# Optimization experiments

Hardware: AMD Instinct MI355X
Metric: run time of the kernel (lower is better)

Reference implementation:

```python
import jax, jax.numpy as jnp
import numpy as np

B, L, IDIM = 1, 1024, 2048
H, DK, DV, K = 16, 128, 128, 4
KEY_DIM = H * DK          # 2048
VAL_DIM = H * DV          # 2048
CONV_DIM = 2 * KEY_DIM + VAL_DIM  # 6144
EPS = 1e-6


def setup_inputs() -> dict:
    key = jax.random.key(0)
    ks = jax.random.split(key, 8)
    s = 0.02
    x = jax.random.normal(ks[0], (B, L, IDIM), jnp.float32)
    Wqkv = jax.random.normal(ks[1], (IDIM, CONV_DIM), jnp.float32) * s
    Wz = jax.random.normal(ks[2], (IDIM, VAL_DIM), jnp.float32) * s
    Wb = jax.random.normal(ks[3], (IDIM, H), jnp.float32) * s
    Wa = jax.random.normal(ks[4], (IDIM, H), jnp.float32) * s
    conv_w = jax.random.normal(ks[5], (CONV_DIM, 1, K), jnp.float32) * 0.2  # depthwise [O,I/g=1,K]
    A_log = jnp.log(jax.random.uniform(ks[6], (H,), jnp.float32, 0.1, 16.0))
    dt_bias = jnp.ones((H,), jnp.float32)
    norm_w = jnp.ones((DV,), jnp.float32)
    Wout = jax.random.normal(ks[7], (VAL_DIM, IDIM), jnp.float32) * s
    return dict(x=x, Wqkv=Wqkv, Wz=Wz, Wb=Wb, Wa=Wa, conv_w=conv_w,
                A_log=A_log, dt_bias=dt_bias, norm_w=norm_w, Wout=Wout)


def _l2norm(t):
    return t * jax.lax.rsqrt(jnp.sum(t * t, axis=-1, keepdims=True) + EPS)


def reference(x, Wqkv, Wz, Wb, Wa, conv_w, A_log, dt_bias, norm_w, Wout):
    b, l, _ = x.shape
    # fused QKV projection + causal depthwise conv + SiLU
    qkv = jnp.einsum('bld,dc->blc', x, Wqkv)                 # [B,L,CONV_DIM]
    qkv = jnp.transpose(qkv, (0, 2, 1))                      # [B,C,L]
    qkv = jax.lax.conv_general_dilated(
        qkv, conv_w, window_strides=(1,), padding=[(K - 1, 0)],
        dimension_numbers=('NCL', 'OIL', 'NCL'), feature_group_count=CONV_DIM)
    qkv = jax.nn.silu(jnp.transpose(qkv, (0, 2, 1)))         # [B,L,C]
    q, k, v = jnp.split(qkv, [KEY_DIM, 2 * KEY_DIM], axis=-1)

    z = jnp.einsum('bld,dv->blv', x, Wz)                     # [B,L,VAL_DIM]
    beta = jax.nn.sigmoid(jnp.einsum('bld,dh->blh', x, Wb))  # [B,L,H]
    A = -jnp.exp(A_log)                                      # [H]
    dt = jax.nn.softplus(jnp.einsum('bld,dh->blh', x, Wa) + dt_bias)
    g = dt * A                                               # [B,L,H] (negative)

    q = _l2norm(q.reshape(b, l, H, DK))
    k = _l2norm(k.reshape(b, l, H, DK))
    v = v.reshape(b, l, H, DV)
    scale = DK ** -0.5

    # time-major for scan: [L,B,H,...]
    qs = jnp.transpose(q, (1, 0, 2, 3)) * scale
    ks_ = jnp.transpose(k, (1, 0, 2, 3))
    vs = jnp.transpose(v, (1, 0, 2, 3))
    bs = jnp.transpose(beta, (1, 0, 2))
    gs = jnp.transpose(g, (1, 0, 2))

    M0 = jnp.zeros((b, H, DK, DV), jnp.float32)

    def step(M, inp):
        q_t, k_t, v_t, b_t, g_t = inp
        M = M * jnp.exp(g_t)[..., None, None]                    # decay
        Mk = jnp.einsum('bhd,bhdv->bhv', k_t, M)                 # readout of old mem
        M = M + jnp.einsum('bhd,bhv->bhdv', k_t, (v_t - Mk) * b_t[..., None])
        o_t = jnp.einsum('bhd,bhdv->bhv', q_t, M)
        return M, o_t

    _, out = jax.lax.scan(step, M0, (qs, ks_, vs, bs, gs))   # out: [L,B,H,DV]
    out = jnp.transpose(out, (1, 0, 2, 3))                   # [B,L,H,DV]

    # RMSNormGated: rms_norm(o) * weight * silu(z)
    zg = z.reshape(b, l, H, DV)
    rms = jax.lax.rsqrt(jnp.mean(out * out, axis=-1, keepdims=True) + EPS)
    out = (out * rms) * norm_w * jax.nn.silu(zg)

    out = out.reshape(b, l, VAL_DIM)
    return jnp.einsum('blv,vd->bld', out, Wout)
```

## Files before the change

### kernel.cpp

```cpp
#include <hip/hip_runtime.h>

typedef short bf16x8 __attribute__((ext_vector_type(8)));
typedef float f32x4 __attribute__((ext_vector_type(4)));
typedef float f32x2 __attribute__((ext_vector_type(2)));
typedef unsigned short u16;
typedef u16 u16x4 __attribute__((ext_vector_type(4)));

#define L_SEQ 1024
#define IDIM_ 2048
#define H_ 16
#define DK_ 128
#define DV_ 128
#define KEYD 2048
#define VALD 2048
#define CONVD 6144
#define QZD 8192
#define CH 16
#define NCH (L_SEQ / CH)
#define SCH 64
#define NSC (L_SEQ / SCH)

__device__ __forceinline__ u16 f2bf(float f) {
  union { float f; unsigned u; } v; v.f = f;
  unsigned r = v.u + 0x7FFF + ((v.u >> 16) & 1);
  return (u16)(r >> 16);
}

__device__ __forceinline__ float red16(float x) {
  union U { float f; int i; } a, t;
  a.f = x;
  t.i = __builtin_amdgcn_update_dpp(0, a.i, 0xB1, 0xF, 0xF, true); a.f += t.f;
  t.i = __builtin_amdgcn_update_dpp(0, a.i, 0x4E, 0xF, 0xF, true); a.f += t.f;
  t.i = __builtin_amdgcn_update_dpp(0, a.i, 0x141, 0xF, 0xF, true); a.f += t.f;
  t.i = __builtin_amdgcn_update_dpp(0, a.i, 0x140, 0xF, 0xF, true); a.f += t.f;
  return a.f;
}

__device__ __forceinline__ void gl_lds16(const float* g, float* l) {
  __builtin_amdgcn_global_load_lds(
      (const __attribute__((address_space(1))) void*)g,
      (__attribute__((address_space(3))) void*)l, 16, 0, 0);
}
__device__ __forceinline__ void gl_lds4(const float* g, float* l) {
  __builtin_amdgcn_global_load_lds(
      (const __attribute__((address_space(1))) void*)g,
      (__attribute__((address_space(3))) void*)l, 4, 0, 0);
}

__global__ __launch_bounds__(256) void prepcast_kernel(const float* __restrict__ x,
                                                       const float* __restrict__ Wqkv,
                                                       const float* __restrict__ Wz,
                                                       const float* __restrict__ Wout,
                                                       u16* __restrict__ xb,
                                                       u16* __restrict__ WcatT,
                                                       u16* __restrict__ WoutT) {
  __shared__ float tile[32][33];
  const int bid = blockIdx.x;
  if (bid < 2048) {
    int i = (bid * 256 + threadIdx.x) * 4;
    f32x4 v = *(const f32x4*)&x[i];
    u16x4 o = { f2bf(v[0]), f2bf(v[1]), f2bf(v[2]), f2bf(v[3]) };
    *(u16x4*)&xb[i] = o;
    return;
  }
  const float* W; u16* WT; int R, C, bx, by;
  if (bid < 14336) {
    int t = bid - 2048;  bx = t % 192; by = t / 192;
    W = Wqkv; WT = WcatT; R = IDIM_; C = CONVD;
  } else if (bid < 18432) {
    int t = bid - 14336; bx = t & 63; by = t >> 6;
    W = Wz; WT = WcatT + (size_t)CONVD * IDIM_; R = IDIM_; C = VALD;
  } else {
    int t = bid - 18432; bx = t & 63; by = t >> 6;
    W = Wout; WT = WoutT; R = VALD; C = IDIM_;
  }
  int c0 = bx * 32, r0 = by * 32;
  int tx = threadIdx.x & 31, ty = threadIdx.x >> 5;
#pragma unroll
  for (int j = 0; j < 4; ++j)
    tile[ty + j * 8][tx] = W[(size_t)(r0 + ty + j * 8) * C + c0 + tx];
  __syncthreads();
#pragma unroll
  for (int j = 0; j < 4; ++j)
    WT[(size_t)(c0 + ty + j * 8) * R + r0 + tx] = f2bf(tile[tx][ty + j * 8]);
}

__global__ __launch_bounds__(256) void gemm_bt_kernel(const u16* __restrict__ A,
                                                      const u16* __restrict__ B,
                                                      float* __restrict__ C,
                                                      int M, int N, int K) {
  __shared__ short As[128 * 72];
  __shared__ short Bs[128 * 72];
  const int tid = threadIdx.x;
  const int lane = tid & 63, wave = tid >> 6;
  const int wm = wave >> 1, wn = wave & 1;
  const int m0 = blockIdx.y * 128, n0 = blockIdx.x * 128;
  const int l15 = lane & 15, lhi = lane >> 4;

  f32x4 acc[4][4] = {};

  for (int k0 = 0; k0 < K; k0 += 64) {
    __syncthreads();
#pragma unroll
    for (int i = 0; i < 4; ++i) {
      int chunk = tid + i * 256;
      int row = chunk >> 3;
      int kc = (chunk & 7) * 8;
      *(bf16x8*)&As[row * 72 + kc] =
          *(const bf16x8*)&A[(size_t)(m0 + row) * K + k0 + kc];
      *(bf16x8*)&Bs[row * 72 + kc] =
          *(const bf16x8*)&B[(size_t)(n0 + row) * K + k0 + kc];
    }
    __syncthreads();
#pragma unroll
    for (int kk = 0; kk < 64; kk += 32) {
      const int koff = kk + lhi * 8;
      bf16x8 a[4], b[4];
#pragma unroll
      for (int m = 0; m < 4; ++m)
        a[m] = *(const bf16x8*)&As[(wm * 64 + m * 16 + l15) * 72 + koff];
#pragma unroll
      for (int n = 0; n < 4; ++n)
        b[n] = *(const bf16x8*)&Bs[(wn * 64 + n * 16 + l15) * 72 + koff];
#pragma unroll
      for (int m = 0; m < 4; ++m)
#pragma unroll
        for (int n = 0; n < 4; ++n)
          acc[m][n] = __builtin_amdgcn_mfma_f32_16x16x32_bf16(a[m], b[n], acc[m][n], 0, 0, 0);
    }
  }
#pragma unroll
  for (int m = 0; m < 4; ++m)
#pragma unroll
    for (int n = 0; n < 4; ++n)
#pragma unroll
      for (int j = 0; j < 4; ++j) {
        int row = m0 + wm * 64 + m * 16 + lhi * 4 + j;
        int col = n0 + wn * 64 + n * 16 + l15;
        C[(size_t)row * N + col] = acc[m][n][j];
      }
}

__global__ __launch_bounds__(256) void gemm_bt64_kernel(const u16* __restrict__ A,
                                                        const u16* __restrict__ B,
                                                        float* __restrict__ C,
                                                        int M, int N, int K) {
  __shared__ short As[64 * 72];
  __shared__ short Bs[128 * 72];
  const int tid = threadIdx.x;
  const int lane = tid & 63, wave = tid >> 6;
  const int wm = wave >> 1, wn = wave & 1;
  const int m0 = blockIdx.y * 64, n0 = blockIdx.x * 128;
  const int l15 = lane & 15, lhi = lane >> 4;

  f32x4 acc[2][4] = {};

  for (int k0 = 0; k0 < K; k0 += 64) {
    __syncthreads();
#pragma unroll
    for (int i = 0; i < 2; ++i) {
      int chunk = tid + i * 256;
      int row = chunk >> 3;
      int kc = (chunk & 7) * 8;
      *(bf16x8*)&As[row * 72 + kc] =
          *(const bf16x8*)&A[(size_t)(m0 + row) * K + k0 + kc];
    }
#pragma unroll
    for (int i = 0; i < 4; ++i) {
      int chunk = tid + i * 256;
      int row = chunk >> 3;
      int kc = (chunk & 7) * 8;
      *(bf16x8*)&Bs[row * 72 + kc] =
          *(const bf16x8*)&B[(size_t)(n0 + row) * K + k0 + kc];
    }
    __syncthreads();
#pragma unroll
    for (int kk = 0; kk < 64; kk += 32) {
      const int koff = kk + lhi * 8;
      bf16x8 a[2], b[4];
#pragma unroll
      for (int m = 0; m < 2; ++m)
        a[m] = *(const bf16x8*)&As[(wm * 32 + m * 16 + l15) * 72 + koff];
#pragma unroll
      for (int n = 0; n < 4; ++n)
        b[n] = *(const bf16x8*)&Bs[(wn * 64 + n * 16 + l15) * 72 + koff];
#pragma unroll
      for (int m = 0; m < 2; ++m)
#pragma unroll
        for (int n = 0; n < 4; ++n)
          acc[m][n] = __builtin_amdgcn_mfma_f32_16x16x32_bf16(a[m], b[n], acc[m][n], 0, 0, 0);
    }
  }
#pragma unroll
  for (int m = 0; m < 2; ++m)
#pragma unroll
    for (int n = 0; n < 4; ++n)
#pragma unroll
      for (int j = 0; j < 4; ++j) {
        int row = m0 + wm * 32 + m * 16 + lhi * 4 + j;
        int col = n0 + wn * 64 + n * 16 + l15;
        C[(size_t)row * N + col] = acc[m][n][j];
      }
}

__global__ __launch_bounds__(128) void betag_kernel(const float* __restrict__ x,
                                                    const float* __restrict__ Wb,
                                                    const float* __restrict__ Wa,
                                                    const float* __restrict__ A_log,
                                                    const float* __restrict__ dt_bias,
                                                    float* __restrict__ btT,
                                                    float* __restrict__ egT,
                                                    float* __restrict__ gT) {
  int l = blockIdx.x;
  __shared__ float xs[IDIM_];
  __shared__ float redb[128], reda[128];
  for (int i = threadIdx.x; i < IDIM_; i += 128) xs[i] = x[(size_t)l * IDIM_ + i];
  __syncthreads();
  int h = threadIdx.x & 15, part = threadIdx.x >> 4;
  float sb = 0.f, sa = 0.f;
  int d0 = part * 256;
  for (int d = d0; d < d0 + 256; ++d) {
    float xv = xs[d];
    sb += xv * Wb[d * 16 + h];
    sa += xv * Wa[d * 16 + h];
  }
  redb[threadIdx.x] = sb;
  reda[threadIdx.x] = sa;
  __syncthreads();
  if (threadIdx.x < 16) {
    float b = 0.f, a = 0.f;
#pragma unroll
    for (int p = 0; p < 8; ++p) { b += redb[p * 16 + h]; a += reda[p * 16 + h]; }
    btT[h * L_SEQ + l] = 1.f / (1.f + expf(-b));
    float dtv = a + dt_bias[h];
    dtv = (dtv > 20.f) ? dtv : log1pf(expf(dtv));
    float g = -expf(A_log[h]) * dtv;
    egT[h * L_SEQ + l] = expf(g);
    gT[h * L_SEQ + l] = g;
  }
}

__global__ __launch_bounds__(256) void prep2_kernel(const float* __restrict__ qkvz,
                                                    const float* __restrict__ cw,
                                                    float* __restrict__ qn,
                                                    float* __restrict__ kn,
                                                    float* __restrict__ vT) {
  __shared__ float tile[32][33];
  const int bid = blockIdx.x;
  if (bid < 4096) {
    int wid = bid * 4 + (threadIdx.x >> 6);
    int lane = threadIdx.x & 63;
    int l = wid >> 4, h = wid & 15;
    const int cq = h * 128 + lane * 2;
    const int ck = KEYD + cq;
    const float* row0 = qkvz + (size_t)l * QZD;
    f32x4 wq0 = *(const f32x4*)&cw[cq * 4];
    f32x4 wq1 = *(const f32x4*)&cw[(cq + 1) * 4];
    f32x4 wk0 = *(const f32x4*)&cw[ck * 4];
    f32x4 wk1 = *(const f32x4*)&cw[(ck + 1) * 4];
    f32x2 xq = *(const f32x2*)&row0[cq];
    f32x2 xk = *(const f32x2*)&row0[ck];
    float q0 = xq[0] * wq0[3], q1 = xq[1] * wq1[3];
    float k0 = xk[0] * wk0[3], k1 = xk[1] * wk1[3];
    if (l >= 1) {
      f32x2 aq = *(const f32x2*)&row0[cq - QZD];
      f32x2 ak = *(const f32x2*)&row0[ck - QZD];
      q0 += aq[0] * wq0[2]; q1 += aq[1] * wq1[2];
      k0 += ak[0] * wk0[2]; k1 += ak[1] * wk1[2];
    }
    if (l >= 2) {
      f32x2 aq = *(const f32x2*)&row0[cq - 2 * QZD];
      f32x2 ak = *(const f32x2*)&row0[ck - 2 * QZD];
      q0 += aq[0] * wq0[1]; q1 += aq[1] * wq1[1];
      k0 += ak[0] * wk0[1]; k1 += ak[1] * wk1[1];
    }
    if (l >= 3) {
      f32x2 aq = *(const f32x2*)&row0[cq - 3 * QZD];
      f32x2 ak = *(const f32x2*)&row0[ck - 3 * QZD];
      q0 += aq[0] * wq0[0]; q1 += aq[1] * wq1[0];
      k0 += ak[0] * wk0[0]; k1 += ak[1] * wk1[0];
    }
    f32x2 qv = { q0 / (1.f + expf(-q0)), q1 / (1.f + expf(-q1)) };
    f32x2 kv = { k0 / (1.f + expf(-k0)), k1 / (1.f + expf(-k1)) };

    float ssq = qv[0] * qv[0] + qv[1] * qv[1];
    float ssk = kv[0] * kv[0] + kv[1] * kv[1];
#pragma unroll
    for (int s = 1; s < 64; s <<= 1) {
      ssq += __shfl_xor(ssq, s);
      ssk += __shfl_xor(ssk, s);
    }
    float scq = 0.08838834764831845f / sqrtf(ssq + 1e-6f);
    float sck = 1.f / sqrtf(ssk + 1e-6f);
    qv[0] *= scq; qv[1] *= scq;
    kv[0] *= sck; kv[1] *= sck;
    size_t base = ((size_t)h * L_SEQ + l) * 128 + lane * 2;
    *(f32x2*)&qn[base] = qv;
    *(f32x2*)&kn[base] = kv;
    return;
  }
  int t = bid - 4096;
  int c0 = (t & 63) * 32, l0 = (t >> 6) * 32;
  int tx = threadIdx.x & 31, ty = threadIdx.x >> 5;
  const int c = 2 * KEYD + c0 + tx;
  f32x4 w = *(const f32x4*)&cw[c * 4];
#pragma unroll
  for (int j = 0; j < 4; ++j) {
    int l = l0 + ty + j * 8;
    const float* p = qkvz + (size_t)l * QZD + c;
    float s = p[0] * w[3];
    if (l >= 1) s += p[-QZD] * w[2];
    if (l >= 2) s += p[-2 * QZD] * w[1];
    if (l >= 3) s += p[-3 * QZD] * w[0];
    tile[ty + j * 8][tx] = s / (1.f + expf(-s));
  }
  __syncthreads();
#pragma unroll
  for (int j = 0; j < 4; ++j)
    vT[(size_t)(c0 + ty + j * 8) * L_SEQ + l0 + tx] = tile[tx][ty + j * 8];
}

__global__ __launch_bounds__(256) void scan_kernel(const float* __restrict__ kn,
                                                   const float* __restrict__ vT,
                                                   const float* __restrict__ egT,
                                                   const float* __restrict__ btT,
                                                   float* __restrict__ Mb,
                                                   float* __restrict__ DbT) {
  __shared__ alignas(16) float ks[2][CH][128];
  __shared__ alignas(16) float vs[2][16][CH];
  __shared__ alignas(16) float ebc[2][2][CH];

  const int tid = threadIdx.x;
  const int wave = tid >> 6, lane = tid & 63;
  const int dk_sub = lane & 15;
  const int head = blockIdx.x & 15;
  const int dv0 = (blockIdx.x >> 4) * 16;
  const int col_local = tid >> 4;
  const int dv = dv0 + col_local;

  const float* kh = kn + (size_t)head * L_SEQ * 128;

  auto stage = [&](int chunk, int buf) {
    const int l0 = chunk * CH;
    const float* kg = kh + (size_t)l0 * 128;
#pragma unroll
    for (int i = 0; i < 2; ++i) {
      int seg = i * 4 + wave;
      int off = seg * 256 + lane * 4;
      gl_lds16(kg + off, &ks[buf][0][0] + seg * 256);
    }
    {
      int idx = wave * 64 + lane;
      gl_lds4(vT + (size_t)(head * 128 + dv0 + (idx >> 4)) * L_SEQ + l0 + (idx & 15),
              &vs[buf][0][0] + wave * 64);
    }
    if (wave == 0 && lane < 32) {
      const float* src = (lane < 16) ? (egT + head * L_SEQ + l0 + lane)
                                     : (btT + head * L_SEQ + l0 + (lane - 16));
      gl_lds4(src, &ebc[buf][0][0]);
    }
  };

  stage(0, 0);
  __syncthreads();

  f32x4 Mlo = {0.f, 0.f, 0.f, 0.f}, Mhi = {0.f, 0.f, 0.f, 0.f};
  const int dkb = dk_sub * 8;
  float* dcol = DbT + (size_t)(head * 128 + dv) * L_SEQ;

#pragma unroll 1
  for (int c = 0; c < NCH; ++c) {
    const int buf = c & 1;
    if (c + 1 < NCH) stage(c + 1, buf ^ 1);

    if ((c & 3) == 0) {
      int sc = c >> 2;
      float* mrow = Mb + (((size_t)sc * 16 + head) * 128 + dv) * 128 + dkb;
      *(f32x4*)mrow = Mlo;
      *(f32x4*)(mrow + 4) = Mhi;
    }

    f32x4 ev[4], bv[4], vv[4];
#pragma unroll
    for (int i = 0; i < 4; ++i) {
      ev[i] = *(const f32x4*)&ebc[buf][0][i * 4];
      bv[i] = *(const f32x4*)&ebc[buf][1][i * 4];
      vv[i] = *(const f32x4*)&vs[buf][col_local][i * 4];
    }
    f32x4 kr[4][2];
#pragma unroll
    for (int i = 0; i < 3; ++i) {
      kr[i][0] = *(const f32x4*)&ks[buf][i][dkb];
      kr[i][1] = *(const f32x4*)&ks[buf][i][dkb + 4];
    }

#pragma unroll
    for (int s = 0; s < CH; ++s) {
      if (s + 3 < CH) {
        kr[(s + 3) & 3][0] = *(const f32x4*)&ks[buf][s + 3][dkb];
        kr[(s + 3) & 3][1] = *(const f32x4*)&ks[buf][s + 3][dkb + 4];
      }
      const f32x4 k0 = kr[s & 3][0], k1 = kr[s & 3][1];
      const float e = ev[s >> 2][s & 3], b = bv[s >> 2][s & 3];
      const float v = vv[s >> 2][s & 3];

      float skm0 = k0[0] * Mlo[0], skm1 = k0[1] * Mlo[1];
      skm0 = fmaf(k0[2], Mlo[2], skm0); skm1 = fmaf(k0[3], Mlo[3], skm1);
      skm0 = fmaf(k1[0], Mhi[0], skm0); skm1 = fmaf(k1[1], Mhi[1], skm1);
      skm0 = fmaf(k1[2], Mhi[2], skm0); skm1 = fmaf(k1[3], Mhi[3], skm1);
      f32x4 emlo, emhi;
#pragma unroll
      for (int i = 0; i < 4; ++i) { emlo[i] = e * Mlo[i]; emhi[i] = e * Mhi[i]; }
      float skm = red16(skm0 + skm1);
      float dl = (v - e * skm) * b;
      if (dk_sub == 0) dcol[c * CH + s] = dl;
#pragma unroll
      for (int i = 0; i < 4; ++i) {
        Mlo[i] = fmaf(k0[i], dl, emlo[i]);
        Mhi[i] = fmaf(k1[i], dl, emhi[i]);
      }
    }
    __syncthreads();
  }
}

__global__ __launch_bounds__(256) void opass_kernel(const float* __restrict__ qn,
                                                    const float* __restrict__ kn,
                                                    const float* __restrict__ DbT,
                                                    const float* __restrict__ gT,
                                                    const float* __restrict__ Mb,
                                                    float* __restrict__ oatt) {
  __shared__ alignas(16) u16 qsb[64][136];
  __shared__ alignas(16) u16 bbuf[128][136];
  __shared__ alignas(16) u16 Asb[64][72];
  __shared__ float gsh[64], Gh[64];

  const int tid = threadIdx.x;
  const int lane = tid & 63, wave = tid >> 6;
  const int l15 = lane & 15, lhi = lane >> 4;
  const int h = blockIdx.x & 15, sc = blockIdx.x >> 4;
  const int l0 = sc * SCH;

  {
    int t = tid >> 2, c0 = (tid & 3) * 32;
    const float* qr = qn + ((size_t)h * L_SEQ + l0 + t) * 128 + c0;
    const float* kr = kn + ((size_t)h * L_SEQ + l0 + t) * 128 + c0;
#pragma unroll
    for (int j = 0; j < 8; ++j) {
      f32x4 vq = *(const f32x4*)&qr[j * 4];
      f32x4 vk = *(const f32x4*)&kr[j * 4];
      u16x4 oq = { f2bf(vq[0]), f2bf(vq[1]), f2bf(vq[2]), f2bf(vq[3]) };
      u16x4 ok = { f2bf(vk[0]), f2bf(vk[1]), f2bf(vk[2]), f2bf(vk[3]) };
      *(u16x4*)&qsb[t][c0 + j * 4] = oq;
      *(u16x4*)&bbuf[t][c0 + j * 4] = ok;
    }
  }
  if (tid < 64) gsh[tid] = gT[h * L_SEQ + l0 + tid];
  __syncthreads();
  if (tid < 64) {
    float a = 0.f;
    for (int u = 0; u <= tid; ++u) a += gsh[u];
    Gh[tid] = a;
  }
  __syncthreads();

  f32x4 acc1[2][2] = {};
  const int wm = wave >> 1, wn = wave & 1;
#pragma unroll
  for (int kk = 0; kk < 128; kk += 32) {
    const int koff = kk + lhi * 8;
    bf16x8 a[2], b[2];
#pragma unroll
    for (int m = 0; m < 2; ++m)
      a[m] = *(const bf16x8*)&qsb[wm * 32 + m * 16 + l15][koff];
#pragma unroll
    for (int n = 0; n < 2; ++n)
      b[n] = *(const bf16x8*)&bbuf[wn * 32 + n * 16 + l15][koff];
#pragma unroll
    for (int m = 0; m < 2; ++m)
#pragma unroll
      for (int n = 0; n < 2; ++n)
        acc1[m][n] = __builtin_amdgcn_mfma_f32_16x16x32_bf16(a[m], b[n], acc1[m][n], 0, 0, 0);
  }
#pragma unroll
  for (int m = 0; m < 2; ++m)
#pragma unroll
    for (int n = 0; n < 2; ++n)
#pragma unroll
      for (int j = 0; j < 4; ++j) {
        int t = wm * 32 + m * 16 + lhi * 4 + j;
        int s = wn * 32 + n * 16 + l15;
        float a = (s <= t) ? acc1[m][n][j] * expf(Gh[t] - Gh[s]) : 0.f;
        Asb[t][s] = f2bf(a);
      }
  __syncthreads();

  {
    int dv = tid >> 1, c0 = (tid & 1) * 64;
    const float* mr = Mb + (((size_t)sc * 16 + h) * 128 + dv) * 128 + c0;
#pragma unroll
    for (int j = 0; j < 16; ++j) {
      f32x4 v = *(const f32x4*)&mr[j * 4];
      u16x4 o = { f2bf(v[0]), f2bf(v[1]), f2bf(v[2]), f2bf(v[3]) };
      *(u16x4*)&bbuf[dv][c0 + j * 4] = o;
    }
  }
  __syncthreads();

  f32x4 acc[2][4] = {};
#pragma unroll
  for (int kk = 0; kk < 128; kk += 32) {
    const int koff = kk + lhi * 8;
    bf16x8 a[2], b[4];
#pragma unroll
    for (int m = 0; m < 2; ++m)
      a[m] = *(const bf16x8*)&qsb[wm * 32 + m * 16 + l15][koff];
#pragma unroll
    for (int n = 0; n < 4; ++n)
      b[n] = *(const bf16x8*)&bbuf[wn * 64 + n * 16 + l15][koff];
#pragma unroll
    for (int m = 0; m < 2; ++m)
#pragma unroll
      for (int n = 0; n < 4; ++n)
        acc[m][n] = __builtin_amdgcn_mfma_f32_16x16x32_bf16(a[m], b[n], acc[m][n], 0, 0, 0);
  }
#pragma unroll
  for (int m = 0; m < 2; ++m) {
#pragma unroll
    for (int j = 0; j < 4; ++j) {
      int t = wm * 32 + m * 16 + lhi * 4 + j;
      float sc1 = expf(Gh[t]);
#pragma unroll
      for (int n = 0; n < 4; ++n) acc[m][n][j] *= sc1;
    }
  }
  __syncthreads();

  {
    int dv = tid >> 1, c0 = (tid & 1) * 32;
    const float* dr = DbT + (size_t)(h * 128 + dv) * L_SEQ + l0 + c0;
#pragma unroll
    for (int j = 0; j < 8; ++j) {
      f32x4 v = *(const f32x4*)&dr[j * 4];
      u16x4 o = { f2bf(v[0]), f2bf(v[1]), f2bf(v[2]), f2bf(v[3]) };
      *(u16x4*)&bbuf[dv][c0 + j * 4] = o;
    }
  }
  __syncthreads();

#pragma unroll
  for (int kk = 0; kk < 64; kk += 32) {
    const int koff = kk + lhi * 8;
    bf16x8 a[2], b[4];
#pragma unroll
    for (int m = 0; m < 2; ++m)
      a[m] = *(const bf16x8*)&Asb[wm * 32 + m * 16 + l15][koff];
#pragma unroll
    for (int n = 0; n < 4; ++n)
      b[n] = *(const bf16x8*)&bbuf[wn * 64 + n * 16 + l15][koff];
#pragma unroll
    for (int m = 0; m < 2; ++m)
#pragma unroll
      for (int n = 0; n < 4; ++n)
        acc[m][n] = __builtin_amdgcn_mfma_f32_16x16x32_bf16(a[m], b[n], acc[m][n], 0, 0, 0);
  }

#pragma unroll
  for (int m = 0; m < 2; ++m)
#pragma unroll
    for (int n = 0; n < 4; ++n)
#pragma unroll
      for (int j = 0; j < 4; ++j) {
        int t = wm * 32 + m * 16 + lhi * 4 + j;
        int dv = wn * 64 + n * 16 + l15;
        oatt[((size_t)(l0 + t) * 16 + h) * 128 + dv] = acc[m][n][j];
      }
}

__global__ __launch_bounds__(256) void grms_kernel(const float* __restrict__ oatt,
                                                   const float* __restrict__ qkvz,
                                                   const float* __restrict__ norm_w,
                                                   u16* __restrict__ gn) {
  int wid = blockIdx.x * 4 + (threadIdx.x >> 6);
  int lane = threadIdx.x & 63;
  int l = wid >> 4, h = wid & 15;
  const float* o = oatt + (size_t)wid * 128;
  f32x2 ov = *(const f32x2*)&o[lane * 2];
  float ss = ov[0] * ov[0] + ov[1] * ov[1];
#pragma unroll
  for (int s = 1; s < 64; s <<= 1) ss += __shfl_xor(ss, s);
  float r = 1.f / sqrtf(ss * (1.f / 128.f) + 1e-6f);
  const float* zp = qkvz + (size_t)l * QZD + CONVD + h * 128;
  f32x2 zv = *(const f32x2*)&zp[lane * 2];
  u16 r0, r1;
  {
    float sil = zv[0] / (1.f + expf(-zv[0]));
    r0 = f2bf(ov[0] * r * norm_w[lane * 2] * sil);
    float sil1 = zv[1] / (1.f + expf(-zv[1]));
    r1 = f2bf(ov[1] * r * norm_w[lane * 2 + 1] * sil1);
  }
  u16* dst = gn + (size_t)l * VALD + h * 128 + lane * 2;
  dst[0] = r0; dst[1] = r1;
}

extern "C" void kernel_launch(void* const* d_in, const int* in_sizes, int n_in,
                              void* d_out, int out_size, void* d_ws, size_t ws_size,
                              hipStream_t stream) {
  const float* x      = (const float*)d_in[0];
  const float* Wqkv   = (const float*)d_in[1];
  const float* Wz     = (const float*)d_in[2];
  const float* Wb     = (const float*)d_in[3];
  const float* Wa     = (const float*)d_in[4];
  const float* conv_w = (const float*)d_in[5];
  const float* A_log  = (const float*)d_in[6];
  const float* dt_bias= (const float*)d_in[7];
  const float* norm_w = (const float*)d_in[8];
  const float* Wout   = (const float*)d_in[9];
  float* out = (float*)d_out;

  char* ws = (char*)d_ws;
  size_t off = 0;
  auto alloc = [&](size_t bytes) {
    void* p = ws + off;
    off = (off + bytes + 255) & ~(size_t)255;
    return p;
  };
  u16* xb     = (u16*)alloc((size_t)L_SEQ * IDIM_ * 2);
  u16* WcatT  = (u16*)alloc((size_t)QZD * IDIM_ * 2);
  u16* WoutT  = (u16*)alloc((size_t)IDIM_ * VALD * 2);
  float* qkvz = (float*)alloc((size_t)L_SEQ * QZD * 4);
  float* qn   = (float*)alloc((size_t)H_ * L_SEQ * 128 * 4);
  float* kn   = (float*)alloc((size_t)H_ * L_SEQ * 128 * 4);
  float* vT   = (float*)alloc((size_t)H_ * 128 * L_SEQ * 4);
  float* btT  = (float*)alloc((size_t)L_SEQ * H_ * 4);
  float* egT  = (float*)alloc((size_t)L_SEQ * H_ * 4);
  float* gTb  = (float*)alloc((size_t)L_SEQ * H_ * 4);
  float* Mb   = (float*)alloc((size_t)NSC * H_ * 128 * 128 * 4);
  float* DbT  = (float*)alloc((size_t)H_ * 128 * L_SEQ * 4);
  float* oatt = (float*)alloc((size_t)L_SEQ * H_ * DV_ * 4);
  u16* gn     = (u16*)alloc((size_t)L_SEQ * VALD * 2);

  prepcast_kernel<<<22528, 256, 0, stream>>>(x, Wqkv, Wz, Wout, xb, WcatT, WoutT);

  gemm_bt_kernel<<<dim3(QZD / 128, L_SEQ / 128), 256, 0, stream>>>(xb, WcatT, qkvz, L_SEQ, QZD, IDIM_);

  betag_kernel<<<L_SEQ, 128, 0, stream>>>(x, Wb, Wa, A_log, dt_bias, btT, egT, gTb);

  prep2_kernel<<<6144, 256, 0, stream>>>(qkvz, conv_w, qn, kn, vT);

  scan_kernel<<<H_ * (DV_ / 16), 256, 0, stream>>>(kn, vT, egT, btT, Mb, DbT);

  opass_kernel<<<NSC * H_, 256, 0, stream>>>(qn, kn, DbT, gTb, Mb, oatt);

  grms_kernel<<<(L_SEQ * H_) / 4, 256, 0, stream>>>(oatt, qkvz, norm_w, gn);
  gemm_bt64_kernel<<<dim3(IDIM_ / 128, L_SEQ / 64), 256, 0, stream>>>(gn, WoutT, out, L_SEQ, IDIM_, VALD);
}
```

Measured before the change: 337.7 us.

## Fuse gated RMSNorm into opass and add XCD-aware GEMM block swizzle

Moves the RMS normalization, SiLU(z) gating and bf16 cast into the epilogue of the output pass, using a wave-level and shared-memory reduction for per-row sums of squares. This removes the separate grms kernel launch and the fp32 oatt round trip through global memory. Both GEMMs now use a 1D grid remapped so that consecutive tiles in N land on the same XCD, aiming for better L2 reuse. The fused epilogue does scattered 2-byte stores and per-element z loads, which may be less coalesced than before.

```diff
diff --git a/kernel.cpp b/kernel.cpp
--- a/kernel.cpp
+++ b/kernel.cpp
@@ -88,13 +88,17 @@
 __global__ __launch_bounds__(256) void gemm_bt_kernel(const u16* __restrict__ A,
                                                       const u16* __restrict__ B,
                                                       float* __restrict__ C,
-                                                      int M, int N, int K) {
+                                                      int M, int N, int K, int cxl) {
   __shared__ short As[128 * 72];
   __shared__ short Bs[128 * 72];
   const int tid = threadIdx.x;
   const int lane = tid & 63, wave = tid >> 6;
   const int wm = wave >> 1, wn = wave & 1;
-  const int m0 = blockIdx.y * 128, n0 = blockIdx.x * 128;
+  const int bid = blockIdx.x;
+  const int xcd = bid & 7, bi = bid >> 3;
+  const int bx = (xcd << cxl) + (bi & ((1 << cxl) - 1));
+  const int by = bi >> cxl;
+  const int m0 = by * 128, n0 = bx * 128;
   const int l15 = lane & 15, lhi = lane >> 4;
 
   f32x4 acc[4][4] = {};
@@ -144,13 +148,17 @@
 __global__ __launch_bounds__(256) void gemm_bt64_kernel(const u16* __restrict__ A,
                                                         const u16* __restrict__ B,
                                                         float* __restrict__ C,
-                                                        int M, int N, int K) {
+                                                        int M, int N, int K, int cxl) {
   __shared__ short As[64 * 72];
   __shared__ short Bs[128 * 72];
   const int tid = threadIdx.x;
   const int lane = tid & 63, wave = tid >> 6;
   const int wm = wave >> 1, wn = wave & 1;
-  const int m0 = blockIdx.y * 64, n0 = blockIdx.x * 128;
+  const int bid = blockIdx.x;
+  const int xcd = bid & 7, bi = bid >> 3;
+  const int bx = (xcd << cxl) + (bi & ((1 << cxl) - 1));
+  const int by = bi >> cxl;
+  const int m0 = by * 64, n0 = bx * 128;
   const int l15 = lane & 15, lhi = lane >> 4;
 
   f32x4 acc[2][4] = {};
@@ -429,11 +437,14 @@
                                                     const float* __restrict__ DbT,
                                                     const float* __restrict__ gT,
                                                     const float* __restrict__ Mb,
-                                                    float* __restrict__ oatt) {
+                                                    const float* __restrict__ qkvz,
+                                                    const float* __restrict__ norm_w,
+                                                    u16* __restrict__ gn) {
   __shared__ alignas(16) u16 qsb[64][136];
   __shared__ alignas(16) u16 bbuf[128][136];
   __shared__ alignas(16) u16 Asb[64][72];
   __shared__ float gsh[64], Gh[64];
+  __shared__ float ssr[2][64];
 
   const int tid = threadIdx.x;
   const int lane = tid & 63, wave = tid >> 6;
@@ -565,42 +576,41 @@
         acc[m][n] = __builtin_amdgcn_mfma_f32_16x16x32_bf16(a[m], b[n], acc[m][n], 0, 0, 0);
   }
 
+  float pr[2][4];
 #pragma unroll
   for (int m = 0; m < 2; ++m)
 #pragma unroll
-    for (int n = 0; n < 4; ++n)
-#pragma unroll
-      for (int j = 0; j < 4; ++j) {
-        int t = wm * 32 + m * 16 + lhi * 4 + j;
+    for (int j = 0; j < 4; ++j) {
+      float p = 0.f;
+#pragma unroll
+      for (int n = 0; n < 4; ++n) p = fmaf(acc[m][n][j], acc[m][n][j], p);
+      pr[m][j] = red16(p);
+    }
+  if (l15 == 0) {
+#pragma unroll
+    for (int m = 0; m < 2; ++m)
+#pragma unroll
+      for (int j = 0; j < 4; ++j)
+        ssr[wn][wm * 32 + m * 16 + lhi * 4 + j] = pr[m][j];
+  }
+  __syncthreads();
+#pragma unroll
+  for (int m = 0; m < 2; ++m)
+#pragma unroll
+    for (int j = 0; j < 4; ++j) {
+      int t = wm * 32 + m * 16 + lhi * 4 + j;
+      float ss = ssr[0][t] + ssr[1][t];
+      float r = 1.f / sqrtf(ss * (1.f / 128.f) + 1e-6f);
+      const float* zp = qkvz + (size_t)(l0 + t) * QZD + CONVD + h * 128;
+      u16* dst = gn + (size_t)(l0 + t) * VALD + h * 128;
+#pragma unroll
+      for (int n = 0; n < 4; ++n) {
         int dv = wn * 64 + n * 16 + l15;
-        oatt[((size_t)(l0 + t) * 16 + h) * 128 + dv] = acc[m][n][j];
+        float z = zp[dv];
+        float sil = z / (1.f + expf(-z));
+        dst[dv] = f2bf(acc[m][n][j] * r * norm_w[dv] * sil);
       }
-}
-
-__global__ __launch_bounds__(256) void grms_kernel(const float* __restrict__ oatt,
-                                                   const float* __restrict__ qkvz,
-                                                   const float* __restrict__ norm_w,
-                                                   u16* __restrict__ gn) {
-  int wid = blockIdx.x * 4 + (threadIdx.x >> 6);
-  int lane = threadIdx.x & 63;
-  int l = wid >> 4, h = wid & 15;
-  const float* o = oatt + (size_t)wid * 128;
-  f32x2 ov = *(const f32x2*)&o[lane * 2];
-  float ss = ov[0] * ov[0] + ov[1] * ov[1];
-#pragma unroll
-  for (int s = 1; s < 64; s <<= 1) ss += __shfl_xor(ss, s);
-  float r = 1.f / sqrtf(ss * (1.f / 128.f) + 1e-6f);
-  const float* zp = qkvz + (size_t)l * QZD + CONVD + h * 128;
-  f32x2 zv = *(const f32x2*)&zp[lane * 2];
-  u16 r0, r1;
-  {
-    float sil = zv[0] / (1.f + expf(-zv[0]));
-    r0 = f2bf(ov[0] * r * norm_w[lane * 2] * sil);
-    float sil1 = zv[1] / (1.f + expf(-zv[1]));
-    r1 = f2bf(ov[1] * r * norm_w[lane * 2 + 1] * sil1);
-  }
-  u16* dst = gn + (size_t)l * VALD + h * 128 + lane * 2;
-  dst[0] = r0; dst[1] = r1;
+    }
 }
 
 extern "C" void kernel_launch(void* const* d_in, const int* in_sizes, int n_in,
@@ -637,12 +647,11 @@
   float* gTb  = (float*)alloc((size_t)L_SEQ * H_ * 4);
   float* Mb   = (float*)alloc((size_t)NSC * H_ * 128 * 128 * 4);
   float* DbT  = (float*)alloc((size_t)H_ * 128 * L_SEQ * 4);
-  float* oatt = (float*)alloc((size_t)L_SEQ * H_ * DV_ * 4);
   u16* gn     = (u16*)alloc((size_t)L_SEQ * VALD * 2);
 
   prepcast_kernel<<<22528, 256, 0, stream>>>(x, Wqkv, Wz, Wout, xb, WcatT, WoutT);
 
-  gemm_bt_kernel<<<dim3(QZD / 128, L_SEQ / 128), 256, 0, stream>>>(xb, WcatT, qkvz, L_SEQ, QZD, IDIM_);
+  gemm_bt_kernel<<<512, 256, 0, stream>>>(xb, WcatT, qkvz, L_SEQ, QZD, IDIM_, 3);
 
   betag_kernel<<<L_SEQ, 128, 0, stream>>>(x, Wb, Wa, A_log, dt_bias, btT, egT, gTb);
 
@@ -650,8 +659,7 @@
 
   scan_kernel<<<H_ * (DV_ / 16), 256, 0, stream>>>(kn, vT, egT, btT, Mb, DbT);
 
-  opass_kernel<<<NSC * H_, 256, 0, stream>>>(qn, kn, DbT, gTb, Mb, oatt);
-
-  grms_kernel<<<(L_SEQ * H_) / 4, 256, 0, stream>>>(oatt, qkvz, norm_w, gn);
-  gemm_bt64_kernel<<<dim3(IDIM_ / 128, L_SEQ / 64), 256, 0, stream>>>(gn, WoutT, out, L_SEQ, IDIM_, VALD);
-}
+  opass_kernel<<<NSC * H_, 256, 0, stream>>>(qn, kn, DbT, gTb, Mb, qkvz, norm_w, gn);
+
+  gemm_bt64_kernel<<<256, 256, 0, stream>>>(gn, WoutT, out, L_SEQ, IDIM_, VALD, 1);
+}
```

Result: no change. 338.3 us (+0.2%).
